# Kernel tuning notes

Hardware: AMD Instinct MI355X
Metric: run time of the kernel (lower is better)

Reference implementation:

```python
import jax, jax.numpy as jnp
import numpy as np

L, N, C = 128, 32, 128
DIM_MLP, OUT = 128, 128


def setup_inputs() -> dict:
    key = jax.random.key(0)
    ks = jax.random.split(key, 6)
    s_in2 = 1.0 / np.sqrt(2 * C)
    s_mid = 1.0 / np.sqrt(DIM_MLP)
    s_in = 1.0 / np.sqrt(C)
    return {
        "x": jax.random.normal(ks[0], (L, N, C), jnp.float32),
        "attn_w1": jax.random.normal(ks[1], (2 * C, DIM_MLP), jnp.float32) * s_in2,
        "attn_b1": jnp.zeros((DIM_MLP,), jnp.float32),
        "attn_w2": jax.random.normal(ks[2], (DIM_MLP, OUT), jnp.float32) * s_mid,
        "attn_b2": jnp.zeros((OUT,), jnp.float32),
        "value_w1": jax.random.normal(ks[3], (C, DIM_MLP), jnp.float32) * s_in,
        "value_b1": jnp.zeros((DIM_MLP,), jnp.float32),
        "value_w2": jax.random.normal(ks[4], (DIM_MLP, OUT), jnp.float32) * s_mid,
        "value_b2": jnp.zeros((OUT,), jnp.float32),
    }


def reference(x, attn_w1, attn_b1, attn_w2, attn_b2,
              value_w1, value_b1, value_w2, value_b2):
    l, n, c = x.shape
    # Outer concat: pair[i, j, b] = concat(x[i, b], x[j, b])  -> (l, l, N, 2C)
    xi = jnp.broadcast_to(x[:, None, :, :], (l, l, n, c))
    xj = jnp.broadcast_to(x[None, :, :, :], (l, l, n, c))
    pair = jnp.concatenate([xi, xj], axis=-1)
    # Pairwise attention MLP (ReLU hidden, linear output)
    h = jax.nn.relu(pair @ attn_w1 + attn_b1)          # (l, l, N, dim_mlp)
    attn = h @ attn_w2 + attn_b2                       # (l, l, N, out)
    # Value MLP
    hv = jax.nn.relu(x @ value_w1 + value_b1)          # (l, N, dim_mlp)
    value = hv @ value_w2 + value_b2                   # (l, N, out)
    # Elementwise weighted reduce over key axis j (NOT a matmul over channels)
    out = jnp.einsum('ijbc,jbc->ibc', attn, value)     # (l, N, out)
    return out
```

## Files before the change

kernel.cpp:

```cpp
#include <hip/hip_runtime.h>
#include <hip/hip_bf16.h>

#define L_DIM 128
#define N_DIM 32
#define C_DIM 128
#define K_DIM 128
#define OUT_DIM 128

typedef __attribute__((ext_vector_type(8))) short short8;
typedef __attribute__((ext_vector_type(4))) float float4v;

static __device__ __forceinline__ short bf16_bits(float f) {
    __bf16 h = (__bf16)f;
    return __builtin_bit_cast(short, h);
}

static __device__ __forceinline__ void gl_lds16(const float* g, float* l) {
    __builtin_amdgcn_global_load_lds(
        (const __attribute__((address_space(1))) unsigned int*)g,
        (__attribute__((address_space(3))) unsigned int*)l, 16, 0, 0);
}

__global__ __launch_bounds__(256) void k_pre(
    const float* __restrict__ x,
    const float* __restrict__ attn_w1, const float* __restrict__ attn_b1,
    const float* __restrict__ attn_w2,
    const float* __restrict__ value_w1, const float* __restrict__ value_b1,
    const float* __restrict__ value_w2, const float* __restrict__ value_b2,
    float* __restrict__ P, float* __restrict__ Q, float* __restrict__ Vt,
    short* __restrict__ W2s)
{
    int bid = blockIdx.x;
    if (bid >= 256) {
        int e = (bid - 256) * 256 + threadIdx.x;
        int idx  = e & 7;
        int colr = (e >> 3) & 15;
        int quad = (e >> 7) & 3;
        int mi   = (e >> 9) & 3;
        int ct   = e >> 11;
        int k = quad * 8 + 32 * mi + idx;
        int c = ct * 16 + colr;
        W2s[e] = bf16_bits(attn_w2[k * OUT_DIM + c]);
        return;
    }

    __shared__ float xs[16][C_DIM];
    __shared__ float hvs[16][K_DIM];
    int tid = threadIdx.x;
    int b   = bid >> 3;
    int i0g = (bid & 7) * 16;

    {
        int f = tid * 8;
        int row = f >> 7, c = f & 127;
        const float* xp = x + ((size_t)(i0g + row) * N_DIM + b) * C_DIM + c;
        *(float4v*)(&xs[row][c])     = *(const float4v*)xp;
        *(float4v*)(&xs[row][c + 4]) = *(const float4v*)(xp + 4);
    }
    __syncthreads();

    int ks   = tid & 127;
    int half = tid >> 7;

    float pacc[8] = {0,0,0,0,0,0,0,0};
    float qacc[8] = {0,0,0,0,0,0,0,0};
    float hacc[8] = {0,0,0,0,0,0,0,0};
    #pragma unroll 4
    for (int c = 0; c < C_DIM; ++c) {
        float wa = attn_w1[c * K_DIM + ks];
        float wb = attn_w1[(C_DIM + c) * K_DIM + ks];
        float wv = value_w1[c * K_DIM + ks];
        #pragma unroll
        for (int r = 0; r < 8; ++r) {
            float xr = xs[half * 8 + r][c];
            pacc[r] = fmaf(xr, wa, pacc[r]);
            qacc[r] = fmaf(xr, wb, qacc[r]);
            hacc[r] = fmaf(xr, wv, hacc[r]);
        }
    }
    float b1 = attn_b1[ks], vb1 = value_b1[ks];
    #pragma unroll
    for (int r = 0; r < 8; ++r) {
        int i = i0g + half * 8 + r;
        P[((size_t)b * L_DIM + i) * K_DIM + ks] = pacc[r];
        Q[((size_t)b * L_DIM + i) * K_DIM + ks] = qacc[r] + b1;
        hvs[half * 8 + r][ks] = fmaxf(hacc[r] + vb1, 0.f);
    }
    __syncthreads();

    float vacc[8] = {0,0,0,0,0,0,0,0};
    #pragma unroll 4
    for (int k = 0; k < K_DIM; ++k) {
        float w = value_w2[k * OUT_DIM + ks];
        #pragma unroll
        for (int r = 0; r < 8; ++r)
            vacc[r] = fmaf(hvs[half * 8 + r][k], w, vacc[r]);
    }
    float vb2 = value_b2[ks];
    float* vp = Vt + ((size_t)b * OUT_DIM + ks) * L_DIM + i0g + half * 8;
    float4v v0 = { vacc[0] + vb2, vacc[1] + vb2, vacc[2] + vb2, vacc[3] + vb2 };
    float4v v1 = { vacc[4] + vb2, vacc[5] + vb2, vacc[6] + vb2, vacc[7] + vb2 };
    *(float4v*)vp       = v0;
    *(float4v*)(vp + 4) = v1;
}

__global__ __launch_bounds__(256)
__attribute__((amdgpu_waves_per_eu(2)))
void k_main(
    const float* __restrict__ P, const float* __restrict__ Q,
    const float* __restrict__ Vt,
    const short* __restrict__ W2s, const float* __restrict__ attn_b2,
    float* __restrict__ out)
{
    __shared__ float P_lds[512];

    int b    = blockIdx.x >> 5;
    int it4  = blockIdx.x & 31;
    int tid  = threadIdx.x;
    int wave = tid >> 6;
    int lane = tid & 63;
    int quad = lane >> 4;
    int col  = lane & 15;
    int ip   = wave >> 1;
    int cth  = wave & 1;

    short8 bfrag[4][4];
    const short8* w2p = (const short8*)W2s;
    #pragma unroll
    for (int cl = 0; cl < 4; ++cl)
        #pragma unroll
        for (int mi = 0; mi < 4; ++mi)
            bfrag[cl][mi] =
                w2p[(((cth * 4 + cl) * 4 + mi) * 4 + quad) * 16 + col];

    if (wave == 0) {
        const float* Pbase = P + ((size_t)b * L_DIM + it4 * 4) * K_DIM;
        gl_lds16(Pbase + lane * 4,       &P_lds[0]);
        gl_lds16(Pbase + 256 + lane * 4, &P_lds[256]);
    }
    __syncthreads();

    const float* qa = Q  + (size_t)b * L_DIM * K_DIM + col * K_DIM + quad * 8;
    const float* va = Vt + (size_t)b * OUT_DIM * L_DIM
                         + (cth * 64 + col) * L_DIM + quad * 4;

    float acc0[4] = {0.f, 0.f, 0.f, 0.f};
    float acc1[4] = {0.f, 0.f, 0.f, 0.f};
    float sv[4]   = {0.f, 0.f, 0.f, 0.f};
    int pofs = 0;

    float4v qreg[2][4][2];
    #pragma unroll
    for (int ksl = 0; ksl < 4; ++ksl) {
        qreg[0][ksl][0] = *(const float4v*)(qa + ksl * 32);
        qreg[0][ksl][1] = *(const float4v*)(qa + ksl * 32 + 4);
    }

    #pragma unroll
    for (int r = 0; r < 8; ++r) {
        asm volatile("" : "+v"(pofs));

        float4v vv[4];
        #pragma unroll
        for (int cl = 0; cl < 4; ++cl)
            vv[cl] = *(const float4v*)(va + (size_t)cl * 16 * L_DIM + r * 16);

        if (r < 7) {
            const float* qn = qa + (r + 1) * 16 * K_DIM;
            #pragma unroll
            for (int ksl = 0; ksl < 4; ++ksl) {
                qreg[(r + 1) & 1][ksl][0] = *(const float4v*)(qn + ksl * 32);
                qreg[(r + 1) & 1][ksl][1] = *(const float4v*)(qn + ksl * 32 + 4);
            }
        }

        short8 af[2][4];
        const float* Pr = &P_lds[(ip * 2) * 128 + quad * 8 + pofs];
        #pragma unroll
        for (int ksl = 0; ksl < 4; ++ksl) {
            float4v q0 = qreg[r & 1][ksl][0];
            float4v q1 = qreg[r & 1][ksl][1];
            #pragma unroll
            for (int ii = 0; ii < 2; ++ii) {
                const float* Pc = Pr + ii * 128 + ksl * 32;
                float4v s0 = *(const float4v*)Pc + q0;
                float4v s1 = *(const float4v*)(Pc + 4) + q1;
                short8 a;
                #pragma unroll
                for (int t = 0; t < 4; ++t) {
                    a[t]     = bf16_bits(fmaxf(s0[t], 0.f));
                    a[t + 4] = bf16_bits(fmaxf(s1[t], 0.f));
                }
                af[ii][ksl] = a;
            }
        }

        #pragma unroll
        for (int cl = 0; cl < 4; ++cl) {
            float4v c40 = {0.f, 0.f, 0.f, 0.f};
            float4v c41 = {0.f, 0.f, 0.f, 0.f};
            #pragma unroll
            for (int ksl = 0; ksl < 4; ++ksl) {
                c40 = __builtin_amdgcn_mfma_f32_16x16x32_bf16(
                        af[0][ksl], bfrag[cl][ksl], c40, 0, 0, 0);
                c41 = __builtin_amdgcn_mfma_f32_16x16x32_bf16(
                        af[1][ksl], bfrag[cl][ksl], c41, 0, 0, 0);
            }
            #pragma unroll
            for (int rr = 0; rr < 4; ++rr) {
                acc0[cl] = fmaf(c40[rr], vv[cl][rr], acc0[cl]);
                acc1[cl] = fmaf(c41[rr], vv[cl][rr], acc1[cl]);
                sv[cl]  += vv[cl][rr];
            }
        }
    }

    #pragma unroll
    for (int cl = 0; cl < 4; ++cl) {
        acc0[cl] += __shfl_xor(acc0[cl], 16, 64);
        acc0[cl] += __shfl_xor(acc0[cl], 32, 64);
        acc1[cl] += __shfl_xor(acc1[cl], 16, 64);
        acc1[cl] += __shfl_xor(acc1[cl], 32, 64);
        sv[cl]   += __shfl_xor(sv[cl], 16, 64);
        sv[cl]   += __shfl_xor(sv[cl], 32, 64);
    }

    if (quad == 0) {
        int i0 = it4 * 4 + ip * 2;
        #pragma unroll
        for (int cl = 0; cl < 4; ++cl) {
            int cc = cth * 64 + cl * 16 + col;
            float bsv = attn_b2[cc] * sv[cl];
            out[((size_t)i0 * N_DIM + b) * OUT_DIM + cc]       = acc0[cl] + bsv;
            out[((size_t)(i0 + 1) * N_DIM + b) * OUT_DIM + cc] = acc1[cl] + bsv;
        }
    }
}

extern "C" void kernel_launch(void* const* d_in, const int* in_sizes, int n_in,
                              void* d_out, int out_size, void* d_ws, size_t ws_size,
                              hipStream_t stream)
{
    const float* x        = (const float*)d_in[0];
    const float* attn_w1  = (const float*)d_in[1];
    const float* attn_b1  = (const float*)d_in[2];
    const float* attn_w2  = (const float*)d_in[3];
    const float* attn_b2  = (const float*)d_in[4];
    const float* value_w1 = (const float*)d_in[5];
    const float* value_b1 = (const float*)d_in[6];
    const float* value_w2 = (const float*)d_in[7];
    const float* value_b2 = (const float*)d_in[8];
    float* out = (float*)d_out;

    float* ws  = (float*)d_ws;
    float* P   = ws;
    float* Q   = ws + 524288;
    float* Vt  = ws + 1048576;
    short* W2s = (short*)(ws + 1572864);

    k_pre<<<320, 256, 0, stream>>>(x, attn_w1, attn_b1, attn_w2,
                                   value_w1, value_b1, value_w2, value_b2,
                                   P, Q, Vt, W2s);
    k_main<<<1024, 256, 0, stream>>>(P, Q, Vt, W2s, attn_b2, out);
}
```

Baseline: 144.8 us.

## Stage Q and V tiles through triple-buffered LDS with async loads

Q and Vt tiles are no longer loaded from global memory into registers per thread. The whole block now stages them into triple-buffered shared memory using async global-to-LDS loads, with explicit vmcnt waits and barriers to pipeline two tiles ahead. V is stored with an XOR swizzle to avoid bank conflicts, and MFMA sections get raised wave priority. The waves_per_eu hint is dropped because LDS use grows to about 50KB per block, which may lower occupancy and adds a barrier each iteration.

Result: faster. 126.4 us (-12.7%).

```diff
diff --git a/kernel.cpp b/kernel.cpp
--- a/kernel.cpp
+++ b/kernel.cpp
@@ -105,13 +105,14 @@
 }
 
 __global__ __launch_bounds__(256)
-__attribute__((amdgpu_waves_per_eu(2)))
 void k_main(
     const float* __restrict__ P, const float* __restrict__ Q,
     const float* __restrict__ Vt,
     const short* __restrict__ W2s, const float* __restrict__ attn_b2,
     float* __restrict__ out)
 {
+    __shared__ float Q_lds[3][2048];
+    __shared__ float V_lds[3][2048];
     __shared__ float P_lds[512];
 
     int b    = blockIdx.x >> 5;
@@ -124,6 +125,9 @@
     int ip   = wave >> 1;
     int cth  = wave & 1;
 
+    const float* Qbase = Q  + (size_t)b * L_DIM * K_DIM;
+    const float* Vbase = Vt + (size_t)b * OUT_DIM * L_DIM;
+
     short8 bfrag[4][4];
     const short8* w2p = (const short8*)W2s;
     #pragma unroll
@@ -132,69 +136,78 @@
         for (int mi = 0; mi < 4; ++mi)
             bfrag[cl][mi] =
                 w2p[(((cth * 4 + cl) * 4 + mi) * 4 + quad) * 16 + col];
+
+    int qsrc[2], vsrc[2];
+    #pragma unroll
+    for (int t = 0; t < 2; ++t) {
+        int n = (t * 4 + wave) * 64 + lane;
+        qsrc[t] = (n & 15) * K_DIM + (n >> 4) * 4;
+        int c = n >> 2, s = n & 3;
+        vsrc[t] = c * L_DIM + ((s ^ (c & 3)) << 2);
+    }
+
+    auto stageQ = [&](int jt, int buf) {
+        #pragma unroll
+        for (int t = 0; t < 2; ++t)
+            gl_lds16(Qbase + jt * 16 * K_DIM + qsrc[t],
+                     &Q_lds[buf][(t * 4 + wave) * 256]);
+    };
+    auto stageV = [&](int jt, int buf) {
+        #pragma unroll
+        for (int t = 0; t < 2; ++t)
+            gl_lds16(Vbase + jt * 16 + vsrc[t],
+                     &V_lds[buf][(t * 4 + wave) * 256]);
+    };
 
     if (wave == 0) {
         const float* Pbase = P + ((size_t)b * L_DIM + it4 * 4) * K_DIM;
         gl_lds16(Pbase + lane * 4,       &P_lds[0]);
         gl_lds16(Pbase + 256 + lane * 4, &P_lds[256]);
     }
-    __syncthreads();
-
-    const float* qa = Q  + (size_t)b * L_DIM * K_DIM + col * K_DIM + quad * 8;
-    const float* va = Vt + (size_t)b * OUT_DIM * L_DIM
-                         + (cth * 64 + col) * L_DIM + quad * 4;
+    stageQ(0, 0); stageV(0, 0);
+    stageQ(1, 1); stageV(1, 1);
+    asm volatile("s_waitcnt vmcnt(4)" ::: "memory");
+    __builtin_amdgcn_sched_barrier(0);
+    __builtin_amdgcn_s_barrier();
 
     float acc0[4] = {0.f, 0.f, 0.f, 0.f};
     float acc1[4] = {0.f, 0.f, 0.f, 0.f};
     float sv[4]   = {0.f, 0.f, 0.f, 0.f};
     int pofs = 0;
 
-    float4v qreg[2][4][2];
-    #pragma unroll
-    for (int ksl = 0; ksl < 4; ++ksl) {
-        qreg[0][ksl][0] = *(const float4v*)(qa + ksl * 32);
-        qreg[0][ksl][1] = *(const float4v*)(qa + ksl * 32 + 4);
-    }
-
     #pragma unroll
     for (int r = 0; r < 8; ++r) {
         asm volatile("" : "+v"(pofs));
 
-        float4v vv[4];
-        #pragma unroll
-        for (int cl = 0; cl < 4; ++cl)
-            vv[cl] = *(const float4v*)(va + (size_t)cl * 16 * L_DIM + r * 16);
-
-        if (r < 7) {
-            const float* qn = qa + (r + 1) * 16 * K_DIM;
+        if (r < 6) { stageQ(r + 2, (r + 2) % 3); stageV(r + 2, (r + 2) % 3); }
+
+        short8 af[2][4];
+        {
+            const float* qb = &Q_lds[r % 3][col * 4];
+            const float* Pr = &P_lds[(ip * 2) * 128 + quad * 8 + pofs];
             #pragma unroll
             for (int ksl = 0; ksl < 4; ++ksl) {
-                qreg[(r + 1) & 1][ksl][0] = *(const float4v*)(qn + ksl * 32);
-                qreg[(r + 1) & 1][ksl][1] = *(const float4v*)(qn + ksl * 32 + 4);
+                int kc0 = (ksl * 4 + quad) * 2;
+                float4v q0 = *(const float4v*)(qb + kc0 * 64);
+                float4v q1 = *(const float4v*)(qb + kc0 * 64 + 64);
+                #pragma unroll
+                for (int ii = 0; ii < 2; ++ii) {
+                    const float* Pc = Pr + ii * 128 + ksl * 32;
+                    float4v s0 = *(const float4v*)Pc + q0;
+                    float4v s1 = *(const float4v*)(Pc + 4) + q1;
+                    short8 a;
+                    #pragma unroll
+                    for (int t = 0; t < 4; ++t) {
+                        a[t]     = bf16_bits(fmaxf(s0[t], 0.f));
+                        a[t + 4] = bf16_bits(fmaxf(s1[t], 0.f));
+                    }
+                    af[ii][ksl] = a;
+                }
             }
         }
 
-        short8 af[2][4];
-        const float* Pr = &P_lds[(ip * 2) * 128 + quad * 8 + pofs];
-        #pragma unroll
-        for (int ksl = 0; ksl < 4; ++ksl) {
-            float4v q0 = qreg[r & 1][ksl][0];
-            float4v q1 = qreg[r & 1][ksl][1];
-            #pragma unroll
-            for (int ii = 0; ii < 2; ++ii) {
-                const float* Pc = Pr + ii * 128 + ksl * 32;
-                float4v s0 = *(const float4v*)Pc + q0;
-                float4v s1 = *(const float4v*)(Pc + 4) + q1;
-                short8 a;
-                #pragma unroll
-                for (int t = 0; t < 4; ++t) {
-                    a[t]     = bf16_bits(fmaxf(s0[t], 0.f));
-                    a[t + 4] = bf16_bits(fmaxf(s1[t], 0.f));
-                }
-                af[ii][ksl] = a;
-            }
-        }
-
+        __builtin_amdgcn_s_setprio(1);
+        const float* Vc = &V_lds[r % 3][0];
         #pragma unroll
         for (int cl = 0; cl < 4; ++cl) {
             float4v c40 = {0.f, 0.f, 0.f, 0.f};
@@ -206,12 +219,23 @@
                 c41 = __builtin_amdgcn_mfma_f32_16x16x32_bf16(
                         af[1][ksl], bfrag[cl][ksl], c41, 0, 0, 0);
             }
+            int cc = cth * 64 + cl * 16 + col;
+            float4v vv = *(const float4v*)
+                (Vc + cc * 16 + ((quad ^ (cc & 3)) << 2));
             #pragma unroll
             for (int rr = 0; rr < 4; ++rr) {
-                acc0[cl] = fmaf(c40[rr], vv[cl][rr], acc0[cl]);
-                acc1[cl] = fmaf(c41[rr], vv[cl][rr], acc1[cl]);
-                sv[cl]  += vv[cl][rr];
+                acc0[cl] = fmaf(c40[rr], vv[rr], acc0[cl]);
+                acc1[cl] = fmaf(c41[rr], vv[rr], acc1[cl]);
+                sv[cl]  += vv[rr];
             }
+        }
+        __builtin_amdgcn_s_setprio(0);
+
+        if (r < 7) {
+            if (r < 6) asm volatile("s_waitcnt vmcnt(4)" ::: "memory");
+            else       asm volatile("s_waitcnt vmcnt(0)" ::: "memory");
+            __builtin_amdgcn_sched_barrier(0);
+            __builtin_amdgcn_s_barrier();
         }
     }
 
```
